# Kernel tuning notes

Measured on AMD Instinct MI355X. Metric: run time of the kernel, lower is better.

The kernel has to match this reference:

```python
import jax, jax.numpy as jnp
import numpy as np

VOCAB, D, B, N = 50000, 256, 512, 8

def setup_inputs() -> dict:
    key = jax.random.key(0)
    ks = jax.random.split(key, 9)
    return {
        "subj_id": jax.random.randint(ks[0], (B, N), 0, VOCAB),
        "subj_w": jax.random.normal(ks[1], (B, N), dtype=jnp.float32),
        "verb_id": jax.random.randint(ks[2], (B, N), 0, VOCAB),
        "verb_w": jax.random.normal(ks[3], (B, N), dtype=jnp.float32),
        "obj_id": jax.random.randint(ks[4], (B, N), 0, VOCAB),
        "obj_w": jax.random.normal(ks[5], (B, N), dtype=jnp.float32),
        "emb": jax.random.normal(ks[6], (VOCAB, D), dtype=jnp.float32),
        "w": jax.random.normal(ks[7], (D, D, D), dtype=jnp.float32) * 0.01,
        "u": jax.random.normal(ks[8], (D, D, D), dtype=jnp.float32) * 0.01,
    }

def reference(subj_id, subj_w, verb_id, verb_w, obj_id, obj_w, emb, w, u):
    # weighted embedding aggregation: (B,N) x (B,N,D) -> (B,D)
    subj = jnp.einsum('bn,bnd->bd', subj_w, emb[subj_id])
    verb = jnp.einsum('bn,bnd->bd', verb_w, emb[verb_id])
    obj = jnp.einsum('bn,bnd->bd', obj_w, emb[obj_id])
    # alpha[c,p,q] = sum_i w[i,p,q] * verb[c,i]
    A = jnp.einsum('ipq,ci->cpq', w, verb)
    # diag(obj) contraction collapses to elementwise scale over p
    G = A * obj[:, :, None]                     # (B, D, D)
    # US[c,p,q] = sum_j u[j,p,q] * subj[c,j]
    US = jnp.einsum('jpq,cj->cpq', u, subj)     # (B, D, D)
    # final[c,q] = sum_p US[c,p,q] * G[c,p,q]
    return jnp.einsum('cpq,cpq->cq', US, G)
```

## Files before the change

kernel.cpp:

```cpp
#include <hip/hip_runtime.h>

#define D 256
#define BATCH 512
#define NTOK 8
#define QT 32
#define PPW 16
#define PAD 10

using f32x4  = __attribute__((ext_vector_type(4))) float;
using bf16x8 = __attribute__((ext_vector_type(8))) short;

__device__ __forceinline__ unsigned short f2bf(float x) {
    unsigned int u = __float_as_uint(x);
    unsigned int r = (u + 0x7fffu + ((u >> 16) & 1u)) >> 16;
    return (unsigned short)r;
}

__global__ __launch_bounds__(256) void prep_kernel(
    const int* __restrict__ subj_id, const float* __restrict__ subj_w,
    const int* __restrict__ verb_id, const float* __restrict__ verb_w,
    const int* __restrict__ obj_id,  const float* __restrict__ obj_w,
    const float* __restrict__ emb,
    unsigned short* __restrict__ verb_pre,
    unsigned short* __restrict__ subj_pre,
    float* __restrict__ objswz,
    float* __restrict__ out)
{
    int c = blockIdx.x;
    int d = threadIdx.x;
    float sv = 0.f, vv = 0.f, ov = 0.f;
#pragma unroll
    for (int n = 0; n < NTOK; ++n) {
        sv += subj_w[c*NTOK+n] * emb[(size_t)subj_id[c*NTOK+n]*D + d];
        vv += verb_w[c*NTOK+n] * emb[(size_t)verb_id[c*NTOK+n]*D + d];
        ov += obj_w [c*NTOK+n] * emb[(size_t)obj_id [c*NTOK+n]*D + d];
    }
    int mtg = c >> 4, r = c & 15;
    int ks = d >> 5, kk = d & 31;
    int lane = ((kk >> 3) << 4) | r;
    int j = kk & 7;
    int idx = ((mtg*8 + ks)*64 + lane)*8 + j;
    verb_pre[idx] = f2bf(vv);
    subj_pre[idx] = f2bf(sv);
    objswz[(size_t)(mtg*D + d)*16 + r] = ov;
    out[(size_t)c*D + d] = 0.f;
}

__global__ __launch_bounds__(512, 2) void main_kernel(
    const float* __restrict__ wmat, const float* __restrict__ umat,
    const unsigned short* __restrict__ verb_pre,
    const unsigned short* __restrict__ subj_pre,
    const float* __restrict__ objswz,
    float* __restrict__ out)
{
    __shared__ unsigned short wT[QT][D + PAD];
    __shared__ unsigned short uT[QT][D + PAD];

    int bid = blockIdx.x;
    int ct  = bid >> 7;
    int grp = bid & 127;
    int qt  = grp >> 4;
    int pc  = grp & 15;
    int q0 = qt * QT;
    int p0 = pc * PPW;

    int tid  = threadIdx.x;
    int wv   = tid >> 6;
    int lane = tid & 63;
    int g    = lane >> 4;
    int r16  = lane & 15;

    int st = tid & 255;
    const float* smat = (tid < 256) ? wmat : umat;
    unsigned short (*sT)[D + PAD] = (tid < 256) ? wT : uT;
    int sa = st >> 3;
    int qc = (st & 7) * 4;

    f32x4 pf[4][2];
#pragma unroll
    for (int m = 0; m < 4; ++m) {
        const f32x4* base = (const f32x4*)(smat + (size_t)(m*64 + sa*2)*(D*D)
                                               + (size_t)p0*D + q0 + qc);
        pf[m][0] = *base;
        pf[m][1] = *(base + (D*D)/4);
    }

    bf16x8 av[2][8], au[2][8];
#pragma unroll
    for (int mt = 0; mt < 2; ++mt) {
        int mtg = ct*16 + wv*2 + mt;
#pragma unroll
        for (int ks = 0; ks < 8; ++ks) {
            size_t off = (size_t)(((mtg*8 + ks)*64) + lane) * 8;
            av[mt][ks] = *(const bf16x8*)(verb_pre + off);
            au[mt][ks] = *(const bf16x8*)(subj_pre + off);
        }
    }

    f32x4 accF[2][2];
#pragma unroll
    for (int mt = 0; mt < 2; ++mt)
#pragma unroll
        for (int nt = 0; nt < 2; ++nt)
            accF[mt][nt] = (f32x4){0.f, 0.f, 0.f, 0.f};

#pragma unroll 1
    for (int pi = 0; pi < PPW; ++pi) {
        __syncthreads();

#pragma unroll
        for (int m = 0; m < 4; ++m) {
            int i0 = m*64 + sa*2;
            f32x4 f0 = pf[m][0];
            f32x4 f1 = pf[m][1];
#pragma unroll
            for (int j = 0; j < 4; ++j) {
                unsigned int v = (unsigned int)f2bf(f0[j])
                               | ((unsigned int)f2bf(f1[j]) << 16);
                *(unsigned int*)&sT[qc+j][i0] = v;
            }
        }

        if (pi + 1 < PPW) {
            int pn = p0 + pi + 1;
#pragma unroll
            for (int m = 0; m < 4; ++m) {
                const f32x4* base = (const f32x4*)(smat + (size_t)(m*64 + sa*2)*(D*D)
                                                       + (size_t)pn*D + q0 + qc);
                pf[m][0] = *base;
                pf[m][1] = *(base + (D*D)/4);
            }
        }
        __syncthreads();

        int p = p0 + pi;
        f32x4 ob[2];
#pragma unroll
        for (int mt = 0; mt < 2; ++mt) {
            int mtg = ct*16 + wv*2 + mt;
            ob[mt] = *(const f32x4*)(objswz + ((size_t)mtg*D + p)*16 + g*4);
        }

#pragma unroll
        for (int nt = 0; nt < 2; ++nt) {
            f32x4 aA[2], aU[2];
#pragma unroll
            for (int mt = 0; mt < 2; ++mt) {
                aA[mt] = (f32x4){0.f, 0.f, 0.f, 0.f};
                aU[mt] = (f32x4){0.f, 0.f, 0.f, 0.f};
            }
#pragma unroll
            for (int ks = 0; ks < 8; ++ks) {
                bf16x8 bw = *(const bf16x8*)&wT[nt*16 + r16][ks*32 + g*8];
                bf16x8 bu = *(const bf16x8*)&uT[nt*16 + r16][ks*32 + g*8];
#pragma unroll
                for (int mt = 0; mt < 2; ++mt) {
                    aA[mt] = __builtin_amdgcn_mfma_f32_16x16x32_bf16(
                        av[mt][ks], bw, aA[mt], 0, 0, 0);
                    aU[mt] = __builtin_amdgcn_mfma_f32_16x16x32_bf16(
                        au[mt][ks], bu, aU[mt], 0, 0, 0);
                }
            }
#pragma unroll
            for (int mt = 0; mt < 2; ++mt)
#pragma unroll
                for (int rr = 0; rr < 4; ++rr)
                    accF[mt][nt][rr] += ob[mt][rr] * aA[mt][rr] * aU[mt][rr];
        }
    }

#pragma unroll
    for (int mt = 0; mt < 2; ++mt)
#pragma unroll
        for (int nt = 0; nt < 2; ++nt)
#pragma unroll
            for (int rr = 0; rr < 4; ++rr) {
                int c = ct*256 + wv*32 + mt*16 + g*4 + rr;
                int q = q0 + nt*16 + r16;
                atomicAdd(&out[(size_t)c*D + q], accF[mt][nt][rr]);
            }
}

extern "C" void kernel_launch(void* const* d_in, const int* in_sizes, int n_in,
                              void* d_out, int out_size, void* d_ws, size_t ws_size,
                              hipStream_t stream) {
    const int*   subj_id = (const int*)  d_in[0];
    const float* subj_w  = (const float*)d_in[1];
    const int*   verb_id = (const int*)  d_in[2];
    const float* verb_w  = (const float*)d_in[3];
    const int*   obj_id  = (const int*)  d_in[4];
    const float* obj_w   = (const float*)d_in[5];
    const float* emb     = (const float*)d_in[6];
    const float* wmat    = (const float*)d_in[7];
    const float* umat    = (const float*)d_in[8];
    float* out = (float*)d_out;

    unsigned short* verb_pre = (unsigned short*)d_ws;
    unsigned short* subj_pre = verb_pre + BATCH*D;
    float* objswz = (float*)((char*)d_ws + 2*BATCH*D*sizeof(unsigned short));

    prep_kernel<<<BATCH, D, 0, stream>>>(subj_id, subj_w, verb_id, verb_w,
                                         obj_id, obj_w, emb,
                                         verb_pre, subj_pre, objswz, out);
    main_kernel<<<256, 512, 0, stream>>>(wmat, umat, verb_pre, subj_pre, objswz, out);
}
```

Baseline: 221.5 us.

## Double-buffer LDS B tiles in MFMA fragment layout with one barrier per step

Replaces the padded transposed LDS tiles with a double-buffered buffer laid out directly in MFMA B-fragment order, so each lane reads its bf16x8 operand contiguously. The next p-slice global loads and the obj scales are issued before the MFMAs, and the bf16 conversion and stores land in the other buffer afterward, leaving one barrier per iteration instead of two. Global loads change from float4 to scalar strided reads, which may hurt coalescing. Occupancy hint drops to one block per CU.

New measurement: 219.4 us. Within noise of the previous version (-0.9%).

```diff
diff --git a/kernel.cpp b/kernel.cpp
--- a/kernel.cpp
+++ b/kernel.cpp
@@ -5,7 +5,6 @@
 #define NTOK 8
 #define QT 32
 #define PPW 16
-#define PAD 10
 
 using f32x4  = __attribute__((ext_vector_type(4))) float;
 using bf16x8 = __attribute__((ext_vector_type(8))) short;
@@ -46,15 +45,14 @@
     out[(size_t)c*D + d] = 0.f;
 }
 
-__global__ __launch_bounds__(512, 2) void main_kernel(
+__global__ __launch_bounds__(512, 1) void main_kernel(
     const float* __restrict__ wmat, const float* __restrict__ umat,
     const unsigned short* __restrict__ verb_pre,
     const unsigned short* __restrict__ subj_pre,
     const float* __restrict__ objswz,
     float* __restrict__ out)
 {
-    __shared__ unsigned short wT[QT][D + PAD];
-    __shared__ unsigned short uT[QT][D + PAD];
+    __shared__ unsigned short Bl[2][8][2][2][64][8];
 
     int bid = blockIdx.x;
     int ct  = bid >> 7;
@@ -70,20 +68,14 @@
     int g    = lane >> 4;
     int r16  = lane & 15;
 
-    int st = tid & 255;
-    const float* smat = (tid < 256) ? wmat : umat;
-    unsigned short (*sT)[D + PAD] = (tid < 256) ? wT : uT;
-    int sa = st >> 3;
-    int qc = (st & 7) * 4;
-
-    f32x4 pf[4][2];
-#pragma unroll
-    for (int m = 0; m < 4; ++m) {
-        const f32x4* base = (const f32x4*)(smat + (size_t)(m*64 + sa*2)*(D*D)
-                                               + (size_t)p0*D + q0 + qc);
-        pf[m][0] = *base;
-        pf[m][1] = *(base + (D*D)/4);
-    }
+    int mat = tid >> 8;
+    int st  = tid & 255;
+    int sq  = st & 31;
+    int cg  = st >> 5;
+    const float* smat = mat ? umat : wmat;
+    const float* sbase = smat + (size_t)(cg*8)*(D*D) + (size_t)p0*D + q0 + sq;
+    int snt = sq >> 4;
+    int sl  = (sq & 15);
 
     bf16x8 av[2][8], au[2][8];
 #pragma unroll
@@ -104,41 +96,50 @@
         for (int nt = 0; nt < 2; ++nt)
             accF[mt][nt] = (f32x4){0.f, 0.f, 0.f, 0.f};
 
+    float pf[4][8];
+
+#pragma unroll
+    for (int m = 0; m < 4; ++m)
+#pragma unroll
+        for (int j = 0; j < 8; ++j)
+            pf[m][j] = sbase[(size_t)(m*64 + j)*(D*D)];
+
+#pragma unroll
+    for (int m = 0; m < 4; ++m) {
+        bf16x8 vv;
+#pragma unroll
+        for (int j = 0; j < 8; ++j) vv[j] = (short)f2bf(pf[m][j]);
+        int c = cg + 8*m;
+        *(bf16x8*)&Bl[0][c >> 2][mat][snt][(c & 3)*16 + sl][0] = vv;
+    }
+
+    f32x4 ob[2];
+#pragma unroll
+    for (int mt = 0; mt < 2; ++mt) {
+        int mtg = ct*16 + wv*2 + mt;
+        ob[mt] = *(const f32x4*)(objswz + ((size_t)mtg*D + p0)*16 + g*4);
+    }
+    __syncthreads();
+
 #pragma unroll 1
     for (int pi = 0; pi < PPW; ++pi) {
-        __syncthreads();
-
-#pragma unroll
-        for (int m = 0; m < 4; ++m) {
-            int i0 = m*64 + sa*2;
-            f32x4 f0 = pf[m][0];
-            f32x4 f1 = pf[m][1];
-#pragma unroll
-            for (int j = 0; j < 4; ++j) {
-                unsigned int v = (unsigned int)f2bf(f0[j])
-                               | ((unsigned int)f2bf(f1[j]) << 16);
-                *(unsigned int*)&sT[qc+j][i0] = v;
-            }
-        }
-
+        int cur = pi & 1;
+        const unsigned short* bufc = &Bl[cur][0][0][0][0][0];
+        unsigned short* bufn = &Bl[cur ^ 1][0][0][0][0][0];
+
+        f32x4 obn[2];
         if (pi + 1 < PPW) {
-            int pn = p0 + pi + 1;
-#pragma unroll
-            for (int m = 0; m < 4; ++m) {
-                const f32x4* base = (const f32x4*)(smat + (size_t)(m*64 + sa*2)*(D*D)
-                                                       + (size_t)pn*D + q0 + qc);
-                pf[m][0] = *base;
-                pf[m][1] = *(base + (D*D)/4);
-            }
-        }
-        __syncthreads();
-
-        int p = p0 + pi;
-        f32x4 ob[2];
-#pragma unroll
-        for (int mt = 0; mt < 2; ++mt) {
-            int mtg = ct*16 + wv*2 + mt;
-            ob[mt] = *(const f32x4*)(objswz + ((size_t)mtg*D + p)*16 + g*4);
+            const float* nb = sbase + (size_t)(pi + 1)*D;
+#pragma unroll
+            for (int m = 0; m < 4; ++m)
+#pragma unroll
+                for (int j = 0; j < 8; ++j)
+                    pf[m][j] = nb[(size_t)(m*64 + j)*(D*D)];
+#pragma unroll
+            for (int mt = 0; mt < 2; ++mt) {
+                int mtg = ct*16 + wv*2 + mt;
+                obn[mt] = *(const f32x4*)(objswz + ((size_t)mtg*D + p0 + pi + 1)*16 + g*4);
+            }
         }
 
 #pragma unroll
@@ -151,8 +152,8 @@
             }
 #pragma unroll
             for (int ks = 0; ks < 8; ++ks) {
-                bf16x8 bw = *(const bf16x8*)&wT[nt*16 + r16][ks*32 + g*8];
-                bf16x8 bu = *(const bf16x8*)&uT[nt*16 + r16][ks*32 + g*8];
+                bf16x8 bw = *(const bf16x8*)(bufc + ((((ks*2 + 0)*2 + nt)*64) + lane)*8);
+                bf16x8 bu = *(const bf16x8*)(bufc + ((((ks*2 + 1)*2 + nt)*64) + lane)*8);
 #pragma unroll
                 for (int mt = 0; mt < 2; ++mt) {
                     aA[mt] = __builtin_amdgcn_mfma_f32_16x16x32_bf16(
@@ -167,6 +168,20 @@
                 for (int rr = 0; rr < 4; ++rr)
                     accF[mt][nt][rr] += ob[mt][rr] * aA[mt][rr] * aU[mt][rr];
         }
+
+        if (pi + 1 < PPW) {
+#pragma unroll
+            for (int m = 0; m < 4; ++m) {
+                bf16x8 vv;
+#pragma unroll
+                for (int j = 0; j < 8; ++j) vv[j] = (short)f2bf(pf[m][j]);
+                int c = cg + 8*m;
+                *(bf16x8*)(bufn + ((((c >> 2)*2 + mat)*2 + snt)*64 + (c & 3)*16 + sl)*8) = vv;
+            }
+            ob[0] = obn[0];
+            ob[1] = obn[1];
+        }
+        __syncthreads();
     }
 
 #pragma unroll
```
